# Optimization experiments

Hardware: AMD Instinct MI355X
Metric: run time of the kernel (lower is better)

The kernel has to match this reference:

```python
import jax, jax.numpy as jnp
import numpy as np

H = W = 128          # input_size
N = 128              # output_size[0] == output_size[1]
B = 64
LIN = (H - 2) * (W - 2)          # 15876
TRI = (N * N + N) // 2           # 8256
TI, TJ = np.triu_indices(N)
TI = jnp.asarray(TI); TJ = jnp.asarray(TJ)


def setup_inputs() -> dict:
    key = jax.random.key(0)
    ks = jax.random.split(key, 7)
    return {
        "x": jax.random.normal(ks[0], (B, 1, H, W), jnp.float32),
        "conv1_w": jax.random.normal(ks[1], (4, 1, 3, 3), jnp.float32) * 0.1,
        "conv1_b": jax.random.normal(ks[2], (4,), jnp.float32) * 0.1,
        "conv2_w": jax.random.normal(ks[3], (1, 4, 1, 1), jnp.float32) * 0.1,
        "conv2_b": jax.random.normal(ks[4], (1,), jnp.float32) * 0.1,
        "out_w": jax.random.normal(ks[5], (TRI, LIN), jnp.float32) * (1.0 / np.sqrt(LIN)),
        "out_b": jax.random.normal(ks[6], (TRI,), jnp.float32) * 0.01,
    }


def reference(x, conv1_w, conv1_b, conv2_w, conv2_b, out_w, out_b):
    dn = ('NCHW', 'OIHW', 'NCHW')
    # conv1 (1->4, 3x3, VALID) + relu
    h = jax.lax.conv_general_dilated(x, conv1_w, (1, 1), 'VALID', dimension_numbers=dn)
    h = jax.nn.relu(h + conv1_b[None, :, None, None])
    # conv2 (4->1, 1x1)
    h = jax.lax.conv_general_dilated(h, conv2_w, (1, 1), 'VALID', dimension_numbers=dn)
    h = h + conv2_b[None, :, None, None]
    # flatten -> linear
    h = h.reshape(x.shape[0], -1)                       # [B, LIN]
    v = h @ out_w.T + out_b                             # [B, TRI]
    # vectorized symmetric triu scatter (replaces per-sample Python loop)
    y = jnp.zeros((x.shape[0], N, N), v.dtype)
    y = y.at[:, TI, TJ].set(v).at[:, TJ, TI].set(v)
    return y[:, None, :, :]                             # [B, 1, N, N]
```

## Files before the change

kernel.cpp:

```cpp
#include <hip/hip_runtime.h>
#include <hip/hip_bf16.h>

#define H_IN   128
#define W_IN   128
#define B_SZ   64
#define CONV_O 126
#define K_DIM  15876
#define N_TRI  8256
#define N_OUT  128
#define BK     32
#define BN     64
#define NSTEPS 497
#define K8     1988
#define KSPLIT 16

typedef short  short8  __attribute__((ext_vector_type(8)));
typedef float  floatx4 __attribute__((ext_vector_type(4)));

__device__ inline short f2bf(float f) {
    union { __hip_bfloat16 h; short s; } u;
    u.h = __float2bfloat16(f);
    return u.s;
}

__global__ __launch_bounds__(256) void conv_kernel(
    const float* __restrict__ x,
    const float* __restrict__ w1,
    const float* __restrict__ b1,
    const float* __restrict__ w2,
    const float* __restrict__ b2,
    unsigned short* __restrict__ hsw)
{
    int t = blockIdx.x * 256 + threadIdx.x;
    int j  = t & 7;
    int m  = (t >> 3) & 63;
    int k8 = t >> 9;
    int p  = k8 * 8 + j;
    float val = 0.f;
    if (p < K_DIM) {
        int oy = p / CONV_O;
        int ox = p - oy * CONV_O;
        const float* xb = x + m * (H_IN * W_IN) + oy * W_IN + ox;
        float xin[9];
#pragma unroll
        for (int dy = 0; dy < 3; ++dy)
#pragma unroll
            for (int dx = 0; dx < 3; ++dx)
                xin[dy * 3 + dx] = xb[dy * W_IN + dx];
        float acc = b2[0];
#pragma unroll
        for (int c = 0; c < 4; ++c) {
            float s = b1[c];
#pragma unroll
            for (int q = 0; q < 9; ++q) s = fmaf(w1[c * 9 + q], xin[q], s);
            s = fmaxf(s, 0.f);
            acc = fmaf(w2[c], s, acc);
        }
        val = acc;
    }
    hsw[t] = (unsigned short)f2bf(val);
}

__global__ __launch_bounds__(256, 4) void gemm_kernel(
    const unsigned short* __restrict__ hsw,
    const float* __restrict__ w,
    float* __restrict__ v)
{
    __shared__ __align__(16) short Bs[64 * 40];

    const int n0    = blockIdx.x * BN;
    const int split = blockIdx.y;
    const int s0 = (NSTEPS * split) / KSPLIT;
    const int s1 = (NSTEPS * (split + 1)) / KSPLIT;

    const int t    = threadIdx.x;
    const int lane = t & 63;
    const int wv   = t >> 6;
    const int quad = lane >> 4;
    const int l16  = lane & 15;

    const int mh = (wv >> 1) * 32;
    const int nq = (wv & 1) * 32;

    const int brow = t >> 2;
    const int bk   = (t & 3) * 8;

    const int boff0 = (nq + l16) * 40 + quad * 8;
    const int boff1 = (nq + 16 + l16) * 40 + quad * 8;

    floatx4 acc00 = {0.f,0.f,0.f,0.f}, acc01 = {0.f,0.f,0.f,0.f};
    floatx4 acc10 = {0.f,0.f,0.f,0.f}, acc11 = {0.f,0.f,0.f,0.f};

    for (int s = s0; s < s1; ++s) {
        const int k0 = s * BK;

        const float* wp = w + (size_t)(n0 + brow) * K_DIM + k0 + bk;
        float bv[8];
        if (k0 + BK <= K_DIM) {
            float4 x0 = *(const float4*)wp;
            float4 x1 = *(const float4*)(wp + 4);
            bv[0]=x0.x; bv[1]=x0.y; bv[2]=x0.z; bv[3]=x0.w;
            bv[4]=x1.x; bv[5]=x1.y; bv[6]=x1.z; bv[7]=x1.w;
        } else {
#pragma unroll
            for (int q = 0; q < 8; ++q)
                bv[q] = (k0 + bk + q < K_DIM) ? wp[q] : 0.f;
        }
        short8 bs;
#pragma unroll
        for (int q = 0; q < 8; ++q) bs[q] = f2bf(bv[q]);

        __syncthreads();
        *(short8*)(Bs + brow * 40 + bk) = bs;
        __syncthreads();

        const unsigned short* ap = hsw + (size_t)(s * 4 + quad) * (64 * 8);
        short8 a0 = *(const short8*)(ap + (mh + l16) * 8);
        short8 a1 = *(const short8*)(ap + (mh + 16 + l16) * 8);
        short8 b0 = *(const short8*)(Bs + boff0);
        short8 b1 = *(const short8*)(Bs + boff1);

        acc00 = __builtin_amdgcn_mfma_f32_16x16x32_bf16(a0, b0, acc00, 0, 0, 0);
        acc01 = __builtin_amdgcn_mfma_f32_16x16x32_bf16(a0, b1, acc01, 0, 0, 0);
        acc10 = __builtin_amdgcn_mfma_f32_16x16x32_bf16(a1, b0, acc10, 0, 0, 0);
        acc11 = __builtin_amdgcn_mfma_f32_16x16x32_bf16(a1, b1, acc11, 0, 0, 0);
    }

    const int nc = n0 + nq + l16;
#pragma unroll
    for (int r = 0; r < 4; ++r) {
        int m = mh + quad * 4 + r;
        atomicAdd(&v[(size_t)m * N_TRI + nc],              acc00[r]);
        atomicAdd(&v[(size_t)m * N_TRI + nc + 16],         acc01[r]);
        atomicAdd(&v[(size_t)(m + 16) * N_TRI + nc],       acc10[r]);
        atomicAdd(&v[(size_t)(m + 16) * N_TRI + nc + 16],  acc11[r]);
    }
}

__global__ __launch_bounds__(256) void scatter_kernel(
    const float* __restrict__ v,
    const float* __restrict__ out_b,
    float* __restrict__ y)
{
    int t = blockIdx.x * 256 + threadIdx.x;
    int b  = t >> 14;
    int ij = t & 16383;
    int i = ij >> 7, j = ij & 127;
    int ii = min(i, j), jj = max(i, j);
    int tri = ii * N_OUT - ((ii * (ii - 1)) >> 1) + (jj - ii);
    y[t] = v[(size_t)b * N_TRI + tri] + out_b[tri];
}

extern "C" void kernel_launch(void* const* d_in, const int* in_sizes, int n_in,
                              void* d_out, int out_size, void* d_ws, size_t ws_size,
                              hipStream_t stream) {
    const float* x   = (const float*)d_in[0];
    const float* c1w = (const float*)d_in[1];
    const float* c1b = (const float*)d_in[2];
    const float* c2w = (const float*)d_in[3];
    const float* c2b = (const float*)d_in[4];
    const float* ow  = (const float*)d_in[5];
    const float* ob  = (const float*)d_in[6];
    float* y = (float*)d_out;

    unsigned short* hsw = (unsigned short*)d_ws;
    float* v = (float*)((char*)d_ws + (size_t)K8 * 64 * 8 * 2);

    hipMemsetAsync(v, 0, (size_t)B_SZ * N_TRI * sizeof(float), stream);

    conv_kernel<<<(K8 * 64 * 8) / 256, 256, 0, stream>>>(x, c1w, c1b, c2w, c2b, hsw);
    gemm_kernel<<<dim3(N_TRI / BN, KSPLIT), 256, 0, stream>>>(hsw, ow, v);
    scatter_kernel<<<(B_SZ * N_OUT * N_OUT) / 256, 256, 0, stream>>>(v, ob, y);
}
```

Baseline: 733.6 us.

## Double-buffer GEMM weight tiles with register prefetch and halve K split

The GEMM loop now prefetches the next step's weight and activation fragments into registers and writes LDS into alternating buffers, so each step needs one barrier instead of two and global loads overlap the MFMAs. KSPLIT drops from 16 to 8, which halves the atomic traffic but leaves fewer blocks. The bias is folded into a new init kernel that replaces the memset, and the scatter kernel no longer adds it. The risks are lower parallelism from the smaller split and extra register pressure from the prefetch.

```diff
diff --git a/kernel.cpp b/kernel.cpp
--- a/kernel.cpp
+++ b/kernel.cpp
@@ -12,7 +12,7 @@
 #define BN     64
 #define NSTEPS 497
 #define K8     1988
-#define KSPLIT 16
+#define KSPLIT 8
 
 typedef short  short8  __attribute__((ext_vector_type(8)));
 typedef float  floatx4 __attribute__((ext_vector_type(4)));
@@ -61,12 +61,22 @@
     hsw[t] = (unsigned short)f2bf(val);
 }
 
+__global__ __launch_bounds__(256) void init_v_kernel(
+    const float* __restrict__ out_b, float* __restrict__ v)
+{
+    int t = blockIdx.x * 256 + threadIdx.x;
+    if (t < B_SZ * N_TRI) {
+        int n = t % N_TRI;
+        v[t] = out_b[n];
+    }
+}
+
 __global__ __launch_bounds__(256, 4) void gemm_kernel(
     const unsigned short* __restrict__ hsw,
     const float* __restrict__ w,
     float* __restrict__ v)
 {
-    __shared__ __align__(16) short Bs[64 * 40];
+    __shared__ __align__(16) short Bs[2][64 * 40];
 
     const int n0    = blockIdx.x * BN;
     const int split = blockIdx.y;
@@ -84,18 +94,19 @@
 
     const int brow = t >> 2;
     const int bk   = (t & 3) * 8;
-
-    const int boff0 = (nq + l16) * 40 + quad * 8;
-    const int boff1 = (nq + 16 + l16) * 40 + quad * 8;
+    const float* wbase = w + (size_t)(n0 + brow) * K_DIM + bk;
+
+    const int aoff0 = (mh + l16) * 8;
+    const int aoff1 = (mh + 16 + l16) * 8;
 
     floatx4 acc00 = {0.f,0.f,0.f,0.f}, acc01 = {0.f,0.f,0.f,0.f};
     floatx4 acc10 = {0.f,0.f,0.f,0.f}, acc11 = {0.f,0.f,0.f,0.f};
 
-    for (int s = s0; s < s1; ++s) {
-        const int k0 = s * BK;
-
-        const float* wp = w + (size_t)(n0 + brow) * K_DIM + k0 + bk;
-        float bv[8];
+    float bv[8];
+    short8 a0, a1;
+    {
+        const int k0 = s0 * BK;
+        const float* wp = wbase + k0;
         if (k0 + BK <= K_DIM) {
             float4 x0 = *(const float4*)wp;
             float4 x1 = *(const float4*)(wp + 4);
@@ -106,24 +117,47 @@
             for (int q = 0; q < 8; ++q)
                 bv[q] = (k0 + bk + q < K_DIM) ? wp[q] : 0.f;
         }
+        const unsigned short* ap = hsw + (size_t)(s0 * 4 + quad) * 512;
+        a0 = *(const short8*)(ap + aoff0);
+        a1 = *(const short8*)(ap + aoff1);
+    }
+
+    for (int s = s0; s < s1; ++s) {
         short8 bs;
 #pragma unroll
         for (int q = 0; q < 8; ++q) bs[q] = f2bf(bv[q]);
+        short* buf = Bs[s & 1];
+        *(short8*)(buf + brow * 40 + bk) = bs;
+
+        const int sn = (s + 1 < s1) ? s + 1 : s;
+        {
+            const int k0n = sn * BK;
+            const float* wp = wbase + k0n;
+            if (k0n + BK <= K_DIM) {
+                float4 x0 = *(const float4*)wp;
+                float4 x1 = *(const float4*)(wp + 4);
+                bv[0]=x0.x; bv[1]=x0.y; bv[2]=x0.z; bv[3]=x0.w;
+                bv[4]=x1.x; bv[5]=x1.y; bv[6]=x1.z; bv[7]=x1.w;
+            } else {
+#pragma unroll
+                for (int q = 0; q < 8; ++q)
+                    bv[q] = (k0n + bk + q < K_DIM) ? wp[q] : 0.f;
+            }
+        }
+        const unsigned short* apn = hsw + (size_t)(sn * 4 + quad) * 512;
+        short8 a0n = *(const short8*)(apn + aoff0);
+        short8 a1n = *(const short8*)(apn + aoff1);
 
         __syncthreads();
-        *(short8*)(Bs + brow * 40 + bk) = bs;
-        __syncthreads();
-
-        const unsigned short* ap = hsw + (size_t)(s * 4 + quad) * (64 * 8);
-        short8 a0 = *(const short8*)(ap + (mh + l16) * 8);
-        short8 a1 = *(const short8*)(ap + (mh + 16 + l16) * 8);
-        short8 b0 = *(const short8*)(Bs + boff0);
-        short8 b1 = *(const short8*)(Bs + boff1);
-
+
+        short8 b0 = *(const short8*)(buf + (nq + l16) * 40 + quad * 8);
+        short8 b1 = *(const short8*)(buf + (nq + 16 + l16) * 40 + quad * 8);
         acc00 = __builtin_amdgcn_mfma_f32_16x16x32_bf16(a0, b0, acc00, 0, 0, 0);
         acc01 = __builtin_amdgcn_mfma_f32_16x16x32_bf16(a0, b1, acc01, 0, 0, 0);
         acc10 = __builtin_amdgcn_mfma_f32_16x16x32_bf16(a1, b0, acc10, 0, 0, 0);
         acc11 = __builtin_amdgcn_mfma_f32_16x16x32_bf16(a1, b1, acc11, 0, 0, 0);
+
+        a0 = a0n; a1 = a1n;
     }
 
     const int nc = n0 + nq + l16;
@@ -139,7 +173,6 @@
 
 __global__ __launch_bounds__(256) void scatter_kernel(
     const float* __restrict__ v,
-    const float* __restrict__ out_b,
     float* __restrict__ y)
 {
     int t = blockIdx.x * 256 + threadIdx.x;
@@ -148,7 +181,7 @@
     int i = ij >> 7, j = ij & 127;
     int ii = min(i, j), jj = max(i, j);
     int tri = ii * N_OUT - ((ii * (ii - 1)) >> 1) + (jj - ii);
-    y[t] = v[(size_t)b * N_TRI + tri] + out_b[tri];
+    y[t] = v[(size_t)b * N_TRI + tri];
 }
 
 extern "C" void kernel_launch(void* const* d_in, const int* in_sizes, int n_in,
@@ -166,9 +199,8 @@
     unsigned short* hsw = (unsigned short*)d_ws;
     float* v = (float*)((char*)d_ws + (size_t)K8 * 64 * 8 * 2);
 
-    hipMemsetAsync(v, 0, (size_t)B_SZ * N_TRI * sizeof(float), stream);
-
     conv_kernel<<<(K8 * 64 * 8) / 256, 256, 0, stream>>>(x, c1w, c1b, c2w, c2b, hsw);
+    init_v_kernel<<<(B_SZ * N_TRI + 255) / 256, 256, 0, stream>>>(ob, v);
     gemm_kernel<<<dim3(N_TRI / BN, KSPLIT), 256, 0, stream>>>(hsw, ow, v);
-    scatter_kernel<<<(B_SZ * N_OUT * N_OUT) / 256, 256, 0, stream>>>(v, ob, y);
-}
+    scatter_kernel<<<(B_SZ * N_OUT * N_OUT) / 256, 256, 0, stream>>>(v, y);
+}
```

Measured after the change: 738.3 us. No clear change (+0.6%).
